# Kernel optimization log

Hardware: AMD Instinct MI355X
Metric: run time of the kernel (lower is better)

Reference implementation:

```python
import jax, jax.numpy as jnp
import numpy as np

D = 768       # model dim
H = 12        # num heads
DH = 64       # hidden_dim per head (D == H*DH)
DT = 32       # time_dim
KTEMP = 1.0   # k_temperature
LN_EPS = 1e-5


def setup_inputs() -> dict:
    key = jax.random.key(0)
    ks = jax.random.split(key, 10)
    B, T = 2, 2048
    states = jax.random.normal(ks[0], (B, T, D), jnp.float32)
    attention_mask = jnp.ones((B, T), jnp.int32)
    s = 0.02
    Wq = jax.random.normal(ks[1], (H * DH, D), jnp.float32) * s
    Wk = jax.random.normal(ks[2], (H * DH, D), jnp.float32) * s
    bk = jax.random.normal(ks[3], (H * DH,), jnp.float32) * s
    Wv = jax.random.normal(ks[4], (H * DH, D), jnp.float32) * s
    bv = jnp.zeros((H * DH,), jnp.float32)           # V.bias zeroed in __init__
    Wo = jax.random.normal(ks[5], (D, H * DH), jnp.float32) * s
    bo = jnp.zeros((D,), jnp.float32)                # O.bias zeroed in __init__
    q_bias = jnp.zeros((H * DH,), jnp.float32)
    time_angle = jax.random.uniform(ks[6], (H, DT), jnp.float32) ** 10 + 1e-8
    head_time_delta = jax.random.uniform(ks[7], (H,), jnp.float32)
    ln_gamma = jnp.ones((D,), jnp.float32)
    ln_beta = jnp.zeros((D,), jnp.float32)
    return {"states": states, "attention_mask": attention_mask,
            "Wq": Wq, "Wk": Wk, "bk": bk, "Wv": Wv, "bv": bv,
            "Wo": Wo, "bo": bo, "q_bias": q_bias,
            "time_angle": time_angle, "head_time_delta": head_time_delta,
            "ln_gamma": ln_gamma, "ln_beta": ln_beta}


def reference(states, attention_mask, Wq, Wk, bk, Wv, bv, Wo, bo, q_bias,
              time_angle, head_time_delta, ln_gamma, ln_beta):
    B, T, _ = states.shape
    dtype = states.dtype
    mask = attention_mask.astype(dtype)[..., None, None]  # B T 1 1

    inv_sqrt_dh = 1.0 / np.sqrt(DH).astype(np.float32)

    def get_time(delta):
        # delta: [1,H,1] or scalar 0.0
        pos = jnp.arange(T, dtype=dtype)[:, None, None]     # T 1 1
        ang = (pos + delta) * time_angle[None]              # T H Dt
        c, s = jnp.cos(ang), jnp.sin(ang)
        return jnp.concatenate([c + s, c - s], axis=-1) * inv_sqrt_dh  # T H 2Dt

    # --- q path ---
    q = states @ Wq.T - jnp.exp(q_bias)                     # B T (H*Dh), Q has no bias
    q = jax.nn.sigmoid(q.reshape(B, T, H, DH)) / DH * mask  # B T H Dh
    time_q = get_time(head_time_delta[None, :, None])       # T H 2Dt (with delta)
    time_k = get_time(0.0)                                  # T H 2Dt
    q_timed = q.sum(-1, keepdims=True) * time_q             # B T H 2Dt
    # scores: B T(query) L(key) H -- the large materialized tensor
    scores = jnp.einsum('bthd,lhd->btlh', q_timed, time_k)

    # --- kv path ---
    k = (states @ Wk.T + bk).reshape(B, T, H, DH) / KTEMP * mask
    v = (states @ Wv.T + bv).reshape(B, T, H, DH)
    kv = jax.nn.softmax(k, axis=-1) * v                     # B T H Dh

    # --- aggregate ---
    loading = jnp.einsum('btlh,blhd->bthd', scores, kv).reshape(B, T, D)
    attn_out = loading @ Wo.T + bo

    # residual + layernorm (dropout is identity in eval)
    x = states + attn_out
    mu = x.mean(-1, keepdims=True)
    var = x.var(-1, keepdims=True)
    return (x - mu) * jax.lax.rsqrt(var + LN_EPS) * ln_gamma + ln_beta
```

## Files before the change

### kernel.cpp

```cpp
#include <hip/hip_runtime.h>
#include <math.h>
#include <stdint.h>

#define TT 2048
#define BB 2
#define DD 768
#define HH 12
#define DHH 64
#define DTT 32
#define NROW 4096

typedef float v4 __attribute__((ext_vector_type(4)));
typedef __attribute__((ext_vector_type(8))) short s8v;
typedef __attribute__((ext_vector_type(4))) float f4v;
typedef unsigned short u16;
typedef __attribute__((ext_vector_type(4))) unsigned short us4;

__device__ __forceinline__ u16 f2bf(float x) {
  unsigned u = __builtin_bit_cast(unsigned, x);
  u += 0x7fffu + ((u >> 16) & 1u);
  return (u16)(u >> 16);
}
__device__ __forceinline__ float bf2f(u16 b) {
  return __builtin_bit_cast(float, (unsigned)b << 16);
}
__device__ __forceinline__ float wave_sum(float v) {
#pragma unroll
  for (int m = 32; m > 0; m >>= 1) v += __shfl_xor(v, m, 64);
  return v;
}
__device__ __forceinline__ void gload16(const void* g, void* l) {
  __builtin_amdgcn_global_load_lds(
      (const __attribute__((address_space(1))) unsigned int*)g,
      (__attribute__((address_space(3))) unsigned int*)l, 16, 0, 0);
}
__device__ __forceinline__ void wait_vm3() {
  asm volatile("s_waitcnt vmcnt(3)" ::: "memory");
  __builtin_amdgcn_sched_barrier(0);
}
__device__ __forceinline__ void wait_vm2() {
  asm volatile("s_waitcnt vmcnt(2)" ::: "memory");
  __builtin_amdgcn_sched_barrier(0);
}
__device__ __forceinline__ void wait_vm0() {
  asm volatile("s_waitcnt vmcnt(0)" ::: "memory");
  __builtin_amdgcn_sched_barrier(0);
}
__device__ __forceinline__ void raw_barrier() {
  asm volatile("s_barrier" ::: "memory");
}
__device__ __forceinline__ int swz_col(int row, int col) {
  int ch = (col >> 3) & 3;
  return (col & ~24) | (((ch ^ ((row >> 1) & 3)) & 3) << 3);
}

__global__ __launch_bounds__(256) void prep(
    const float* __restrict__ tang, const float* __restrict__ hdelta,
    const float* __restrict__ s, const float* __restrict__ wq,
    const float* __restrict__ wk, const float* __restrict__ wv,
    const float* __restrict__ wo, u16* __restrict__ timeqb,
    u16* __restrict__ timekb, u16* __restrict__ sb, u16* __restrict__ wqb,
    u16* __restrict__ wkvb, u16* __restrict__ wob) {
  int bid = blockIdx.x;
  if (bid < 192) {
    int idx = bid * 256 + threadIdx.x;
    int d = idx & 31;
    int h = (idx >> 5) % HH;
    int tc = idx / (32 * HH);
    int t0 = tc * 16;
    float ang = tang[h * DTT + d];
    float ca, sa;
    sincosf(ang, &sa, &ca);
    float ck, sk, cq, sq;
    sincosf((float)t0 * ang, &sk, &ck);
    sincosf(((float)t0 + hdelta[h]) * ang, &sq, &cq);
#pragma unroll
    for (int j = 0; j < 16; ++j) {
      int t = t0 + j;
      timekb[t * DD + h * DHH + d]       = f2bf((ck + sk) * 0.125f);
      timekb[t * DD + h * DHH + d + DTT] = f2bf((ck - sk) * 0.125f);
      timeqb[t * DD + h * DHH + d]       = f2bf((cq + sq) * 0.125f);
      timeqb[t * DD + h * DHH + d + DTT] = f2bf((cq - sq) * 0.125f);
      float ck2 = ck * ca - sk * sa;
      sk = sk * ca + ck * sa;
      ck = ck2;
      float cq2 = cq * ca - sq * sa;
      sq = sq * ca + cq * sa;
      cq = cq2;
    }
    return;
  }
  int idx = (bid - 192) * 256 + threadIdx.x;
  int off = idx * 4;
  const float* src;
  u16* dst;
  int so, rr, cc;
  if (off < 3145728) {
    src = s; dst = sb; so = off; rr = so / 768; cc = so % 768;
  } else if (off < 3735552) {
    src = wq; dst = wqb; so = off - 3145728; rr = so / 768; cc = so % 768;
  } else if (off < 4325376) {
    src = wk; so = off - 3735552;
    int j = so / 768; cc = so - j * 768;
    int h = j >> 6, r = j & 63;
    dst = wkvb; rr = h * 128 + r;
  } else if (off < 4915200) {
    src = wv; so = off - 4325376;
    int j = so / 768; cc = so - j * 768;
    int h = j >> 6, r = j & 63;
    dst = wkvb; rr = h * 128 + 64 + r;
  } else {
    src = wo; dst = wob; so = off - 4915200; rr = so / 768; cc = so % 768;
  }
  int dof = rr * 768 + swz_col(rr, cc);
  v4 f = *(const v4*)&src[so];
  us4 o;
#pragma unroll
  for (int j = 0; j < 4; ++j) o[j] = f2bf(f[j]);
  *(us4*)&dst[dof] = o;
}

__global__ __launch_bounds__(256) void gemm_qkv_fused(
    const u16* __restrict__ A, const u16* __restrict__ Wqb,
    const u16* __restrict__ Wkvb, const float* __restrict__ qb,
    const float* __restrict__ bk, const float* __restrict__ bv,
    const int* __restrict__ amask, float* __restrict__ qsum,
    u16* __restrict__ kvb) {
  __shared__ __align__(16) u16 As[3][2176];
  __shared__ __align__(16) u16 Bs[3][4096];
  const int tid = threadIdx.x;
  const int l = tid & 63;
  const int w = tid >> 6;
  const int wr = w >> 1, wc = w & 1;
  const int bx = blockIdx.x;
  const bool isQ = bx < 6;
  const int i0 = blockIdx.y * 64;
  const u16* Bbase = isQ ? (Wqb + (size_t)bx * 128 * 768)
                         : (Wkvb + (size_t)(bx - 6) * 128 * 768);
  const int srow = tid >> 2, scol = (tid & 3) * 8;
  const u16* gA0 = A + (size_t)(i0 + srow) * 768 + scol;
  const u16* gB0 = Bbase + (size_t)srow * 768 + scol;
  const u16* gB1 = gB0 + (size_t)64 * 768;
  const int lo = tid * 8;
  f4v acc[2][4];
#pragma unroll
  for (int m = 0; m < 2; ++m)
#pragma unroll
    for (int n = 0; n < 4; ++n) acc[m][n] = (f4v){0.f, 0.f, 0.f, 0.f};

#define STAGE(kt, b)                       \
  do {                                     \
    int kb_ = (kt) << 5;                   \
    gload16(gA0 + kb_, &As[b][lo]);        \
    gload16(gB0 + kb_, &Bs[b][lo]);        \
    gload16(gB1 + kb_, &Bs[b][2048 + lo]); \
  } while (0)

  STAGE(0, 0);
  STAGE(1, 1);
  int aoff[2], boff[4];
#pragma unroll
  for (int m = 0; m < 2; ++m) {
    int row = wr * 32 + (l & 15) + m * 16;
    aoff[m] = row * 32 + (((l >> 4) ^ ((row >> 1) & 3)) << 3);
  }
#pragma unroll
  for (int n = 0; n < 4; ++n) {
    int row = wc * 64 + (l & 15) + n * 16;
    boff[n] = row * 32 + (((l >> 4) ^ ((row >> 1) & 3)) << 3);
  }
  int cb = 0;
  for (int kt = 0; kt < 24; ++kt) {
    if (kt < 23) wait_vm3();
    else wait_vm0();
    raw_barrier();
    if (kt + 2 < 24) STAGE(kt + 2, (cb + 2) % 3);
    s8v af[2], bf4[4];
#pragma unroll
    for (int m = 0; m < 2; ++m) af[m] = *(const s8v*)&As[cb][aoff[m]];
#pragma unroll
    for (int n = 0; n < 4; ++n) bf4[n] = *(const s8v*)&Bs[cb][boff[n]];
#pragma unroll
    for (int m = 0; m < 2; ++m)
#pragma unroll
      for (int n = 0; n < 4; ++n)
        acc[m][n] =
            __builtin_amdgcn_mfma_f32_16x16x32_bf16(af[m], bf4[n], acc[m][n], 0, 0, 0);
    cb = (cb == 2) ? 0 : cb + 1;
  }
  __syncthreads();

  const int crow = i0 + wr * 32 + (l >> 4) * 4;
  if (isQ) {
    const int head = bx * 2 + wc;
    float eqb[4];
#pragma unroll
    for (int n = 0; n < 4; ++n)
      eqb[n] = expf(qb[head * 64 + n * 16 + (l & 15)]);
#pragma unroll
    for (int m = 0; m < 2; ++m)
#pragma unroll
      for (int r = 0; r < 4; ++r) {
        float ssum = 0.f;
#pragma unroll
        for (int n = 0; n < 4; ++n)
          ssum += 1.f / (1.f + expf(-(acc[m][n][r] - eqb[n])));
#pragma unroll
        for (int mm = 8; mm > 0; mm >>= 1) ssum += __shfl_xor(ssum, mm, 64);
        int row = crow + m * 16 + r;
        if ((l & 15) == 0)
          qsum[row * HH + head] = ssum * (float)amask[row] * (1.f / 64.f);
      }
  } else {
    const int head = bx - 6;
    u16* Ps = &As[0][0];
    if (wc == 0) {
#pragma unroll
      for (int m = 0; m < 2; ++m)
#pragma unroll
        for (int r = 0; r < 4; ++r) {
          int row = crow + m * 16 + r;
          float mk = (float)amask[row];
          float kv4[4];
#pragma unroll
          for (int n = 0; n < 4; ++n)
            kv4[n] = (acc[m][n][r] + bk[head * 64 + n * 16 + (l & 15)]) * mk;
          float mx = fmaxf(fmaxf(kv4[0], kv4[1]), fmaxf(kv4[2], kv4[3]));
#pragma unroll
          for (int mm = 8; mm > 0; mm >>= 1)
            mx = fmaxf(mx, __shfl_xor(mx, mm, 64));
          float e[4], es = 0.f;
#pragma unroll
          for (int n = 0; n < 4; ++n) { e[n] = expf(kv4[n] - mx); es += e[n]; }
#pragma unroll
          for (int mm = 8; mm > 0; mm >>= 1) es += __shfl_xor(es, mm, 64);
          float inv = 1.f / es;
          int lrow = wr * 32 + (l >> 4) * 4 + m * 16 + r;
#pragma unroll
          for (int n = 0; n < 4; ++n)
            Ps[lrow * 68 + n * 16 + (l & 15)] = f2bf(e[n] * inv);
        }
    }
    __syncthreads();
    if (wc == 1) {
#pragma unroll
      for (int m = 0; m < 2; ++m)
#pragma unroll
        for (int r = 0; r < 4; ++r) {
          int row = crow + m * 16 + r;
          int lrow = wr * 32 + (l >> 4) * 4 + m * 16 + r;
#pragma unroll
          for (int n = 0; n < 4; ++n) {
            int d = n * 16 + (l & 15);
            float p = bf2f(Ps[lrow * 68 + d]);
            float vv = acc[m][n][r] + bv[head * 64 + d];
            kvb[((size_t)row * HH + head) * 64 + d] = f2bf(p * vv);
          }
        }
    }
  }
}

__global__ __launch_bounds__(256) void calc_M(
    const u16* __restrict__ timekb, const u16* __restrict__ kvb,
    float* __restrict__ Mpart) {
  int blk = blockIdx.x;
  int split = blk & 31;
  int bh = blk >> 5;
  int b = bh / HH, h = bh % HH;
  __shared__ float Tk[64][68];
  __shared__ float Kv[64][68];
  int tid = threadIdx.x;
  int tx = tid & 15, ty = tid >> 4;
  float acc[4][4] = {};
  int t0 = split * 64;
#pragma unroll
  for (int p = 0; p < 4; ++p) {
    int f = tid + 256 * p;
    int r = f >> 4, c4 = (f & 15) << 2;
    int t = t0 + r;
    us4 tk = *(const us4*)&timekb[(size_t)t * DD + h * DHH + c4];
    us4 kv = *(const us4*)&kvb[((size_t)(b * TT + t) * HH + h) * 64 + c4];
#pragma unroll
    for (int j = 0; j < 4; ++j) {
      Tk[r][c4 + j] = bf2f(tk[j]);
      Kv[r][c4 + j] = bf2f(kv[j]);
    }
  }
  __syncthreads();
#pragma unroll
  for (int kk = 0; kk < 64; ++kk) {
    v4 a = *(const v4*)&Tk[kk][ty * 4];
    v4 bv4 = *(const v4*)&Kv[kk][tx * 4];
#pragma unroll
    for (int r = 0; r < 4; ++r)
#pragma unroll
      for (int c = 0; c < 4; ++c) acc[r][c] += a[r] * bv4[c];
  }
#pragma unroll
  for (int r = 0; r < 4; ++r)
#pragma unroll
    for (int c = 0; c < 4; ++c)
      Mpart[(size_t)blk * 4096 + (tx * 4 + c) * 64 + (ty * 4 + r)] = acc[r][c];
}

__global__ __launch_bounds__(256) void reduce_M(
    const float* __restrict__ Mpart, u16* __restrict__ Mtb) {
  int idx = blockIdx.x * 256 + threadIdx.x;
  int bh = idx >> 12;
  int p = idx & 4095;
  float s = 0.f;
#pragma unroll
  for (int sp = 0; sp < 32; ++sp)
    s += Mpart[(size_t)((bh << 5) + sp) * 4096 + p];
  Mtb[(size_t)bh * 4096 + p] = f2bf(s);
}

__global__ __launch_bounds__(256) void calc_loading_mfma(
    const u16* __restrict__ timeqb, const u16* __restrict__ Mtb,
    const float* __restrict__ qsum, u16* __restrict__ loading) {
  const int bh = blockIdx.y;
  const int b = bh / HH, h = bh % HH;
  const int t0 = blockIdx.x * 64;
  __shared__ __align__(16) u16 Ms[64 * 72];
  for (int p = threadIdx.x; p < 4096; p += 256)
    Ms[(p >> 6) * 72 + (p & 63)] = Mtb[(size_t)bh * 4096 + p];
  __syncthreads();
  const int l = threadIdx.x & 63, w = threadIdx.x >> 6;
  f4v acc[4];
#pragma unroll
  for (int n = 0; n < 4; ++n) acc[n] = (f4v){0.f, 0.f, 0.f, 0.f};
  const int arow = t0 + w * 16 + (l & 15);
  const int dcol = l & 15;
#pragma unroll
  for (int ks = 0; ks < 2; ++ks) {
    const int k0 = ks * 32 + (l >> 4) * 8;
    s8v af, bf4[4];
    af = *(const s8v*)&timeqb[(size_t)arow * DD + h * DHH + k0];
#pragma unroll
    for (int n = 0; n < 4; ++n)
      bf4[n] = *(const s8v*)&Ms[(dcol + n * 16) * 72 + k0];
#pragma unroll
    for (int n = 0; n < 4; ++n)
      acc[n] = __builtin_amdgcn_mfma_f32_16x16x32_bf16(af, bf4[n], acc[n], 0, 0, 0);
  }
  const int trow = t0 + w * 16 + (l >> 4) * 4;
  float qs[4];
#pragma unroll
  for (int r = 0; r < 4; ++r)
    qs[r] = qsum[(b * TT + trow + r) * HH + h];
#pragma unroll
  for (int n = 0; n < 4; ++n)
#pragma unroll
    for (int r = 0; r < 4; ++r) {
      int i = b * TT + trow + r;
      int col = h * DHH + n * 16 + (l & 15);
      loading[(size_t)i * DD + swz_col(i, col)] = f2bf(qs[r] * acc[n][r]);
    }
}

__global__ __launch_bounds__(256) void gemm_out(
    const u16* __restrict__ A, const u16* __restrict__ B, float* __restrict__ C,
    const float* __restrict__ bias, const float* __restrict__ res) {
  __shared__ __align__(16) u16 As[3][2048];
  __shared__ __align__(16) u16 Bs[3][2048];
  const int tid = threadIdx.x;
  const int l = tid & 63;
  const int w = tid >> 6;
  const int wr = w >> 1, wc = w & 1;
  const int i0 = blockIdx.y * 64, j0 = blockIdx.x * 64;
  const int srow = tid >> 2, scol = (tid & 3) * 8;
  const u16* gA0 = A + (size_t)(i0 + srow) * 768 + scol;
  const u16* gB0 = B + (size_t)(j0 + srow) * 768 + scol;
  const int lo = tid * 8;
  f4v acc[2][2];
#pragma unroll
  for (int m = 0; m < 2; ++m)
#pragma unroll
    for (int n = 0; n < 2; ++n) acc[m][n] = (f4v){0.f, 0.f, 0.f, 0.f};

#define STAGE2(kt, b)                 \
  do {                                \
    int kb_ = (kt) << 5;              \
    gload16(gA0 + kb_, &As[b][lo]);   \
    gload16(gB0 + kb_, &Bs[b][lo]);   \
  } while (0)

  STAGE2(0, 0);
  STAGE2(1, 1);
  int aoff[2], boff[2];
#pragma unroll
  for (int m = 0; m < 2; ++m) {
    int row = wr * 32 + (l & 15) + m * 16;
    aoff[m] = row * 32 + (((l >> 4) ^ ((row >> 1) & 3)) << 3);
  }
#pragma unroll
  for (int n = 0; n < 2; ++n) {
    int row = wc * 32 + (l & 15) + n * 16;
    boff[n] = row * 32 + (((l >> 4) ^ ((row >> 1) & 3)) << 3);
  }
  int cb = 0;
  for (int kt = 0; kt < 24; ++kt) {
    if (kt < 23) wait_vm2();
    else wait_vm0();
    raw_barrier();
    if (kt + 2 < 24) STAGE2(kt + 2, (cb + 2) % 3);
    s8v af[2], bf4[2];
#pragma unroll
    for (int m = 0; m < 2; ++m) af[m] = *(const s8v*)&As[cb][aoff[m]];
#pragma unroll
    for (int n = 0; n < 2; ++n) bf4[n] = *(const s8v*)&Bs[cb][boff[n]];
#pragma unroll
    for (int m = 0; m < 2; ++m)
#pragma unroll
      for (int n = 0; n < 2; ++n)
        acc[m][n] =
            __builtin_amdgcn_mfma_f32_16x16x32_bf16(af[m], bf4[n], acc[m][n], 0, 0, 0);
    cb = (cb == 2) ? 0 : cb + 1;
  }
  const int crow = i0 + wr * 32 + (l >> 4) * 4;
  const int ccol = j0 + wc * 32 + (l & 15);
#pragma unroll
  for (int m = 0; m < 2; ++m)
#pragma unroll
    for (int n = 0; n < 2; ++n) {
      int col = ccol + n * 16;
      size_t base = (size_t)(crow + m * 16) * 768 + col;
#pragma unroll
      for (int r = 0; r < 2 * 2; ++r)
        if (r < 4)
          C[base + (size_t)r * 768] =
              acc[m][n][r] + bias[col] + res[base + (size_t)r * 768];
    }
}

__global__ __launch_bounds__(256) void layernorm(
    const float* __restrict__ X, const float* __restrict__ gamma,
    const float* __restrict__ beta, float* __restrict__ out) {
  int i = blockIdx.x;
  const float* x = X + (size_t)i * 768;
  float vals[3];
  float s = 0.f, s2 = 0.f;
#pragma unroll
  for (int p = 0; p < 3; ++p) {
    float v = x[threadIdx.x + 256 * p];
    vals[p] = v;
    s += v;
    s2 += v * v;
  }
  s = wave_sum(s);
  s2 = wave_sum(s2);
  __shared__ float red[8];
  int w = threadIdx.x >> 6;
  if ((threadIdx.x & 63) == 0) {
    red[w] = s;
    red[4 + w] = s2;
  }
  __syncthreads();
  float stot = red[0] + red[1] + red[2] + red[3];
  float s2tot = red[4] + red[5] + red[6] + red[7];
  float mu = stot * (1.f / 768.f);
  float var = s2tot * (1.f / 768.f) - mu * mu;
  float rs = rsqrtf(var + 1e-5f);
#pragma unroll
  for (int p = 0; p < 3; ++p) {
    int j = threadIdx.x + 256 * p;
    out[(size_t)i * 768 + j] = (vals[p] - mu) * rs * gamma[j] + beta[j];
  }
}

extern "C" void kernel_launch(void* const* d_in, const int* in_sizes, int n_in,
                              void* d_out, int out_size, void* d_ws,
                              size_t ws_size, hipStream_t stream) {
  const float* states = (const float*)d_in[0];
  const int* amask    = (const int*)d_in[1];
  const float* Wq     = (const float*)d_in[2];
  const float* Wk     = (const float*)d_in[3];
  const float* bk     = (const float*)d_in[4];
  const float* Wv     = (const float*)d_in[5];
  const float* bv     = (const float*)d_in[6];
  const float* Wo     = (const float*)d_in[7];
  const float* bo     = (const float*)d_in[8];
  const float* qb     = (const float*)d_in[9];
  const float* tang   = (const float*)d_in[10];
  const float* hdelta = (const float*)d_in[11];
  const float* gamma  = (const float*)d_in[12];
  const float* beta   = (const float*)d_in[13];
  float* out = (float*)d_out;
  float* ws = (float*)d_ws;

  u16* timeqb = (u16*)(ws + 0);
  u16* timekb = (u16*)(ws + 786432);
  u16* Abf    = (u16*)(ws + 1572864);
  u16* Wqb    = (u16*)(ws + 3145728);
  u16* Wkvb   = (u16*)(ws + 3440640);
  u16* Wob    = (u16*)(ws + 4030464);
  float* qsum = ws + 4325376;
  u16* kvb    = (u16*)(ws + 4374528);
  float* Mpart= ws + 5160960;
  u16* Mtb    = (u16*)(ws + 8306688);
  u16* loadb  = (u16*)(ws + 8331264);
  float* xbuf = ws + 9117696;

  prep<<<5568, 256, 0, stream>>>(tang, hdelta, states, Wq, Wk, Wv, Wo, timeqb,
                                 timekb, Abf, Wqb, Wkvb, Wob);
  gemm_qkv_fused<<<dim3(18, 64), 256, 0, stream>>>(Abf, Wqb, Wkvb, qb, bk, bv,
                                                   amask, qsum, kvb);
  calc_M<<<768, 256, 0, stream>>>(timekb, kvb, Mpart);
  reduce_M<<<384, 256, 0, stream>>>(Mpart, Mtb);
  calc_loading_mfma<<<dim3(32, 24), 256, 0, stream>>>(timeqb, Mtb, qsum, loadb);
  gemm_out<<<dim3(12, 64), 256, 0, stream>>>(loadb, Wob, xbuf, bo, states);
  layernorm<<<4096, 256, 0, stream>>>(xbuf, gamma, beta, out);
}
```

Baseline: 94.35 us.

## Widen QKV GEMM tile to 64x256 with double-buffered LDS pipeline

Each block of the fused QKV GEMM now computes a 64x256 output tile instead of 64x128. All four waves share the same A rows, and each wave owns one 64-column slice, so there are 4x4 MFMA accumulators per wave. The 3-stage LDS ring becomes a 2-stage double buffer, with an extra barrier before each refill. This halves the grid (1152 to 576 blocks) to cut redundant A-tile loads and raise MFMA reuse per LDS read, at the cost of more registers, more LDS, fewer blocks to fill the CUs, and less prefetch depth.

```diff
diff --git a/kernel.cpp b/kernel.cpp
--- a/kernel.cpp
+++ b/kernel.cpp
@@ -34,8 +34,8 @@
       (const __attribute__((address_space(1))) unsigned int*)g,
       (__attribute__((address_space(3))) unsigned int*)l, 16, 0, 0);
 }
-__device__ __forceinline__ void wait_vm3() {
-  asm volatile("s_waitcnt vmcnt(3)" ::: "memory");
+__device__ __forceinline__ void wait_vm5() {
+  asm volatile("s_waitcnt vmcnt(5)" ::: "memory");
   __builtin_amdgcn_sched_barrier(0);
 }
 __device__ __forceinline__ void wait_vm2() {
@@ -126,79 +126,80 @@
     const float* __restrict__ bk, const float* __restrict__ bv,
     const int* __restrict__ amask, float* __restrict__ qsum,
     u16* __restrict__ kvb) {
-  __shared__ __align__(16) u16 As[3][2176];
-  __shared__ __align__(16) u16 Bs[3][4096];
+  __shared__ __align__(16) u16 As[2][2048];
+  __shared__ __align__(16) u16 Bs[2][8192];
   const int tid = threadIdx.x;
   const int l = tid & 63;
   const int w = tid >> 6;
-  const int wr = w >> 1, wc = w & 1;
   const int bx = blockIdx.x;
-  const bool isQ = bx < 6;
+  const bool isQ = bx < 3;
   const int i0 = blockIdx.y * 64;
-  const u16* Bbase = isQ ? (Wqb + (size_t)bx * 128 * 768)
-                         : (Wkvb + (size_t)(bx - 6) * 128 * 768);
+  const u16* Bbase = isQ ? (Wqb + (size_t)bx * 256 * 768)
+                         : (Wkvb + (size_t)(bx - 3) * 256 * 768);
   const int srow = tid >> 2, scol = (tid & 3) * 8;
   const u16* gA0 = A + (size_t)(i0 + srow) * 768 + scol;
   const u16* gB0 = Bbase + (size_t)srow * 768 + scol;
-  const u16* gB1 = gB0 + (size_t)64 * 768;
   const int lo = tid * 8;
-  f4v acc[2][4];
-#pragma unroll
-  for (int m = 0; m < 2; ++m)
+  f4v acc[4][4];
+#pragma unroll
+  for (int m = 0; m < 4; ++m)
 #pragma unroll
     for (int n = 0; n < 4; ++n) acc[m][n] = (f4v){0.f, 0.f, 0.f, 0.f};
 
-#define STAGE(kt, b)                       \
-  do {                                     \
-    int kb_ = (kt) << 5;                   \
-    gload16(gA0 + kb_, &As[b][lo]);        \
-    gload16(gB0 + kb_, &Bs[b][lo]);        \
-    gload16(gB1 + kb_, &Bs[b][2048 + lo]); \
+#define STAGE(kt, b)                                          \
+  do {                                                        \
+    int kb_ = (kt) << 5;                                      \
+    gload16(gA0 + kb_, &As[b][lo]);                           \
+    gload16(gB0 + kb_, &Bs[b][lo]);                           \
+    gload16(gB0 + kb_ + 64 * 768, &Bs[b][2048 + lo]);         \
+    gload16(gB0 + kb_ + 128 * 768, &Bs[b][4096 + lo]);        \
+    gload16(gB0 + kb_ + 192 * 768, &Bs[b][6144 + lo]);        \
   } while (0)
 
   STAGE(0, 0);
   STAGE(1, 1);
-  int aoff[2], boff[4];
-#pragma unroll
-  for (int m = 0; m < 2; ++m) {
-    int row = wr * 32 + (l & 15) + m * 16;
+  int aoff[4], boff[4];
+#pragma unroll
+  for (int m = 0; m < 4; ++m) {
+    int row = (l & 15) + m * 16;
     aoff[m] = row * 32 + (((l >> 4) ^ ((row >> 1) & 3)) << 3);
   }
 #pragma unroll
   for (int n = 0; n < 4; ++n) {
-    int row = wc * 64 + (l & 15) + n * 16;
+    int row = w * 64 + (l & 15) + n * 16;
     boff[n] = row * 32 + (((l >> 4) ^ ((row >> 1) & 3)) << 3);
   }
   int cb = 0;
   for (int kt = 0; kt < 24; ++kt) {
-    if (kt < 23) wait_vm3();
+    if (kt < 23) wait_vm5();
     else wait_vm0();
     raw_barrier();
-    if (kt + 2 < 24) STAGE(kt + 2, (cb + 2) % 3);
-    s8v af[2], bf4[4];
-#pragma unroll
-    for (int m = 0; m < 2; ++m) af[m] = *(const s8v*)&As[cb][aoff[m]];
+    s8v af[4], bf4[4];
+#pragma unroll
+    for (int m = 0; m < 4; ++m) af[m] = *(const s8v*)&As[cb][aoff[m]];
 #pragma unroll
     for (int n = 0; n < 4; ++n) bf4[n] = *(const s8v*)&Bs[cb][boff[n]];
 #pragma unroll
-    for (int m = 0; m < 2; ++m)
+    for (int m = 0; m < 4; ++m)
 #pragma unroll
       for (int n = 0; n < 4; ++n)
         acc[m][n] =
             __builtin_amdgcn_mfma_f32_16x16x32_bf16(af[m], bf4[n], acc[m][n], 0, 0, 0);
-    cb = (cb == 2) ? 0 : cb + 1;
+    raw_barrier();
+    if (kt + 2 < 24) STAGE(kt + 2, cb);
+    cb ^= 1;
   }
   __syncthreads();
 
-  const int crow = i0 + wr * 32 + (l >> 4) * 4;
+  const int crow = i0 + (l >> 4) * 4;
   if (isQ) {
-    const int head = bx * 2 + wc;
+    const int head = bx * 4 + w;
     float eqb[4];
 #pragma unroll
     for (int n = 0; n < 4; ++n)
       eqb[n] = expf(qb[head * 64 + n * 16 + (l & 15)]);
 #pragma unroll
-    for (int m = 0; m < 2; ++m)
+    for (int m = 0; m < 4; ++m)
 #pragma unroll
       for (int r = 0; r < 4; ++r) {
         float ssum = 0.f;
@@ -212,11 +213,12 @@
           qsum[row * HH + head] = ssum * (float)amask[row] * (1.f / 64.f);
       }
   } else {
-    const int head = bx - 6;
-    u16* Ps = &As[0][0];
-    if (wc == 0) {
-#pragma unroll
-      for (int m = 0; m < 2; ++m)
+    const int hloc = w >> 1;
+    const int head = (bx - 3) * 2 + hloc;
+    u16* Ps = &Bs[0][0] + hloc * 4352;
+    if ((w & 1) == 0) {
+#pragma unroll
+      for (int m = 0; m < 4; ++m)
 #pragma unroll
         for (int r = 0; r < 4; ++r) {
           int row = crow + m * 16 + r;
@@ -235,20 +237,20 @@
 #pragma unroll
           for (int mm = 8; mm > 0; mm >>= 1) es += __shfl_xor(es, mm, 64);
           float inv = 1.f / es;
-          int lrow = wr * 32 + (l >> 4) * 4 + m * 16 + r;
+          int lrow = (l >> 4) * 4 + m * 16 + r;
 #pragma unroll
           for (int n = 0; n < 4; ++n)
             Ps[lrow * 68 + n * 16 + (l & 15)] = f2bf(e[n] * inv);
         }
     }
     __syncthreads();
-    if (wc == 1) {
-#pragma unroll
-      for (int m = 0; m < 2; ++m)
+    if ((w & 1) == 1) {
+#pragma unroll
+      for (int m = 0; m < 4; ++m)
 #pragma unroll
         for (int r = 0; r < 4; ++r) {
           int row = crow + m * 16 + r;
-          int lrow = wr * 32 + (l >> 4) * 4 + m * 16 + r;
+          int lrow = (l >> 4) * 4 + m * 16 + r;
 #pragma unroll
           for (int n = 0; n < 4; ++n) {
             int d = n * 16 + (l & 15);
@@ -427,10 +429,9 @@
       int col = ccol + n * 16;
       size_t base = (size_t)(crow + m * 16) * 768 + col;
 #pragma unroll
-      for (int r = 0; r < 2 * 2; ++r)
-        if (r < 4)
-          C[base + (size_t)r * 768] =
-              acc[m][n][r] + bias[col] + res[base + (size_t)r * 768];
+      for (int r = 0; r < 4; ++r)
+        C[base + (size_t)r * 768] =
+            acc[m][n][r] + bias[col] + res[base + (size_t)r * 768];
     }
 }
 
@@ -504,8 +505,8 @@
 
   prep<<<5568, 256, 0, stream>>>(tang, hdelta, states, Wq, Wk, Wv, Wo, timeqb,
                                  timekb, Abf, Wqb, Wkvb, Wob);
-  gemm_qkv_fused<<<dim3(18, 64), 256, 0, stream>>>(Abf, Wqb, Wkvb, qb, bk, bv,
-                                                   amask, qsum, kvb);
+  gemm_qkv_fused<<<dim3(9, 64), 256, 0, stream>>>(Abf, Wqb, Wkvb, qb, bk, bv,
+                                                  amask, qsum, kvb);
   calc_M<<<768, 256, 0, stream>>>(timekb, kvb, Mpart);
   reduce_M<<<384, 256, 0, stream>>>(Mpart, Mtb);
   calc_loading_mfma<<<dim3(32, 24), 256, 0, stream>>>(timeqb, Mtb, qsum, loadb);
```

New measurement: 102.3 us. +8.4%, slower.
